# Optimization experiments

Hardware: AMD Instinct MI355X
Metric: run time of the kernel (lower is better)

Reference implementation:

```python
import jax, jax.numpy as jnp
import numpy as np

N_EMB = 1024
EMB_DIM = 256
BETA = 0.25


def setup_inputs() -> dict:
    key = jax.random.key(0)
    k1, k2 = jax.random.split(key)
    z = jax.random.normal(k1, (32, EMB_DIM, 32, 32), dtype=jnp.float32)
    init = 1.0 / N_EMB
    emb = jax.random.uniform(k2, (N_EMB, EMB_DIM), dtype=jnp.float32,
                             minval=-init, maxval=init)
    return {"z": z, "emb": emb}


def reference(z, emb):
    # z: [B, C, H, W] -> [B, H, W, C]
    zc = jnp.transpose(z, (0, 2, 3, 1))
    z_flat = zc.reshape(-1, EMB_DIM)  # [N, D]

    # squared L2 distances: ||z||^2 + ||e||^2 - 2 z.e^T  -> [N, K]
    distances = (jnp.sum(z_flat ** 2, axis=1, keepdims=True)
                 + jnp.sum(emb ** 2, axis=1)
                 - 2.0 * (z_flat @ emb.T))
    nearest_idx = jnp.argmin(distances, axis=1)           # [N]
    nearest = jax.nn.one_hot(nearest_idx, N_EMB, dtype=jnp.float32)  # [N, K]

    # direct gather == one-hot matmul, same math
    zq = emb[nearest_idx].reshape(zc.shape)               # [B, H, W, C]

    loss = (jnp.mean((jax.lax.stop_gradient(zq) - zc) ** 2)
            + BETA * jnp.mean((zq - jax.lax.stop_gradient(zc)) ** 2))

    # straight-through estimator
    zq_st = zc + jax.lax.stop_gradient(zq - zc)

    e_mean = jnp.mean(nearest, axis=0)                    # [K]
    perplexity = jnp.exp(-jnp.sum(e_mean * jnp.log(e_mean + 1e-10)))

    zq_out = jnp.transpose(zq_st, (0, 3, 1, 2))           # back to NCHW
    return zq_out, loss, perplexity, nearest, nearest_idx[:, None]
```

## Files before the change

### kernel.cpp

```cpp
#include <hip/hip_runtime.h>

#define N_EMB  1024
#define EMB_D  256
#define HW     1024

#define OUT_ZQ      0
#define OUT_LOSS    8388608
#define OUT_PERP    8388609
#define OUT_NEAREST 8388610
#define OUT_IDX     41943042

#define WS_HIST   0
#define WS_ESQ    4096
#define WS_LOSSP  8192
#define WS_EH     16384
#define WS_TOTAL  540672

typedef unsigned long long ull;
typedef _Float16 half8 __attribute__((ext_vector_type(8)));
typedef float f32x4 __attribute__((ext_vector_type(4)));
typedef ull ull2 __attribute__((ext_vector_type(2)));

#define L_A     0
#define L_B     16384
#define L_ESQ   32768
#define L_ZSQ   36864
#define L_WIN   36992
#define L_RED   37120
#define L_TOT   39168

__device__ __forceinline__ void gload16(const void* g, void* l) {
    __builtin_amdgcn_global_load_lds(
        (const __attribute__((address_space(1))) unsigned int*)g,
        (__attribute__((address_space(3))) unsigned int*)l, 16, 0, 0);
}

__device__ __forceinline__ float pairwise8_combine(const float r[8]) {
    return __fadd_rn(__fadd_rn(__fadd_rn(r[0], r[1]), __fadd_rn(r[2], r[3])),
                     __fadd_rn(__fadd_rn(r[4], r[5]), __fadd_rn(r[6], r[7])));
}

__global__ void prep(const float* __restrict__ emb, _Float16* __restrict__ eh,
                     float* __restrict__ esq, int* __restrict__ hist) {
    int bid = blockIdx.x;
    if (bid < 1024) {
        int c = bid, k = threadIdx.x;
        eh[c * EMB_D + k] = (_Float16)emb[c * EMB_D + k];
        return;
    }
    int c = (bid - 1024) * 256 + threadIdx.x;
    const float* p = emb + (size_t)c * EMB_D;
    float tot[2];
    #pragma unroll
    for (int h = 0; h < 2; ++h) {
        float r[8];
        #pragma unroll
        for (int i = 0; i < 8; ++i) {
            float x = p[h * 128 + i];
            r[i] = __fmul_rn(x, x);
        }
        for (int k = 8; k < 128; k += 8) {
            #pragma unroll
            for (int i = 0; i < 8; ++i) {
                float x = p[h * 128 + k + i];
                r[i] = __fadd_rn(r[i], __fmul_rn(x, x));
            }
        }
        tot[h] = pairwise8_combine(r);
    }
    esq[c] = __fadd_rn(tot[0], tot[1]);
    hist[c] = 0;
}

__global__ __launch_bounds__(256, 4) void fused_vq(
        const float* __restrict__ z, const float* __restrict__ emb,
        const _Float16* __restrict__ eh, const float* __restrict__ esq,
        float* __restrict__ out, int* __restrict__ hist,
        double* __restrict__ lossp) {
    __shared__ __align__(16) char lds[L_TOT];
    int t = threadIdx.x, bid = blockIdx.x;
    int b = bid >> 5, hw0 = (bid & 31) << 5;
    int lane = t & 63, wave = t >> 6;
    int wm = wave >> 1, wn = wave & 1;
    int l15 = lane & 15, lq = lane >> 4;

    if (t < 64) {
        int nl = t & 31, h = (t >> 5) & 1;
        const float* zp = z + ((size_t)b << 18) + hw0 + nl;
        int kb = h << 7;
        int abase = L_A + nl * 512;
        int sw = (nl & 7) << 4;
        float r[8];
        {   half8 hv;
            #pragma unroll
            for (int e = 0; e < 8; ++e) {
                float x = zp[(size_t)(kb + e) << 10];
                hv[e] = (_Float16)x;
                r[e] = __fmul_rn(x, x);
            }
            *(half8*)(lds + abase + (((kb << 1)) ^ sw)) = hv;
        }
        for (int c8 = 1; c8 < 16; ++c8) {
            half8 hv;
            #pragma unroll
            for (int e = 0; e < 8; ++e) {
                float x = zp[(size_t)(kb + c8 * 8 + e) << 10];
                hv[e] = (_Float16)x;
                r[e] = __fadd_rn(r[e], __fmul_rn(x, x));
            }
            *(half8*)(lds + abase + (((kb << 1) + c8 * 16) ^ sw)) = hv;
        }
        *(float*)(lds + L_RED + (h * 32 + nl) * 4) = pairwise8_combine(r);
    } else if (t >= 128) {
        int i = t - 128;
        #pragma unroll
        for (int q = 0; q < 2; ++q) {
            f32x4 v = *(const f32x4*)(esq + (q * 128 + i) * 4);
            *(f32x4*)(lds + L_ESQ + (q * 128 + i) * 16) = v;
        }
    }
    __syncthreads();
    if (t < 32) {
        float t0 = *(float*)(lds + L_RED + t * 4);
        float t1 = *(float*)(lds + L_RED + 128 + t * 4);
        *(float*)(lds + L_ZSQ + t * 4) = __fadd_rn(t0, t1);
    }
    __syncthreads();

    int aoffs[2], boffs[4][2];
    {
        int r = wm * 16 + l15;
        #pragma unroll
        for (int kc = 0; kc < 2; ++kc)
            aoffs[kc] = L_A + r * 512 + ((kc * 64 + lq * 16) ^ ((r & 7) << 4));
    }
    #pragma unroll
    for (int j = 0; j < 4; ++j) {
        int c = wn * 64 + j * 16 + l15;
        #pragma unroll
        for (int kc = 0; kc < 2; ++kc)
            boffs[j][kc] = L_B + c * 128 + ((kc * 64 + lq * 16) ^ ((c & 7) << 4));
    }
    int bsrc[4], bdst[4];
    #pragma unroll
    for (int is = 0; is < 4; ++is) {
        int o = is * 4096 + t * 16;
        int col = o >> 7;
        int K = (o & 127) ^ ((col & 7) << 4);
        bsrc[is] = col * 256 + (K >> 1);
        bdst[is] = L_B + o;
    }
    float zs[4];
    #pragma unroll
    for (int s = 0; s < 4; ++s)
        zs[s] = *(const float*)(lds + L_ZSQ + (wm * 16 + lq * 4 + s) * 4);
    ull k1[4], k2[4];
    #pragma unroll
    for (int s = 0; s < 4; ++s) { k1[s] = ~0ULL; k2[s] = ~0ULL; }

    for (int cbt = 0; cbt < 8; ++cbt) {
        f32x4 acc[4];
        #pragma unroll
        for (int j = 0; j < 4; ++j) acc[j] = (f32x4){0.f, 0.f, 0.f, 0.f};

        for (int kt = 0; kt < 4; ++kt) {
            __syncthreads();
            #pragma unroll
            for (int is = 0; is < 4; ++is)
                gload16(eh + cbt * 32768 + kt * 64 + bsrc[is], lds + bdst[is]);
            __syncthreads();

            half8 a0 = *(const half8*)(lds + aoffs[0] + kt * 128);
            half8 a1 = *(const half8*)(lds + aoffs[1] + kt * 128);
            half8 bb[4][2];
            #pragma unroll
            for (int j = 0; j < 4; ++j) {
                bb[j][0] = *(const half8*)(lds + boffs[j][0]);
                bb[j][1] = *(const half8*)(lds + boffs[j][1]);
            }
            #pragma unroll
            for (int j = 0; j < 4; ++j) {
                acc[j] = __builtin_amdgcn_mfma_f32_16x16x32_f16(a0, bb[j][0], acc[j], 0, 0, 0);
                acc[j] = __builtin_amdgcn_mfma_f32_16x16x32_f16(a1, bb[j][1], acc[j], 0, 0, 0);
            }
        }
        float es[4];
        #pragma unroll
        for (int j = 0; j < 4; ++j)
            es[j] = *(const float*)(lds + L_ESQ + ((cbt << 7) + wn * 64 + j * 16 + l15) * 4);
        #pragma unroll
        for (int s = 0; s < 4; ++s) {
            float zsv = zs[s];
            #pragma unroll
            for (int j = 0; j < 4; ++j) {
                float d = __fsub_rn(__fadd_rn(zsv, es[j]), __fmul_rn(2.0f, acc[j][s]));
                int cg = (cbt << 7) + wn * 64 + j * 16 + l15;
                ull key = ((ull)__float_as_uint(d) << 32) | (unsigned)cg;
                if (key < k1[s]) { k2[s] = k1[s]; k1[s] = key; }
                else if (key < k2[s]) { k2[s] = key; }
            }
        }
    }

    __syncthreads();
    #pragma unroll
    for (int s = 0; s < 4; ++s) {
        int row = wm * 16 + lq * 4 + s;
        *(ull2*)(lds + L_A + row * 512 + ((wn << 4) + l15) * 16) = (ull2){k1[s], k2[s]};
    }
    __syncthreads();

    for (int rr = 0; rr < 8; ++rr) {
        int row = wave * 8 + rr;
        ull k = *(const ull*)(lds + L_A + row * 512 + lane * 8);
        ull kmin = k;
        #pragma unroll
        for (int m = 1; m < 64; m <<= 1) {
            ull o = __shfl_xor(kmin, m, 64);
            kmin = o < kmin ? o : kmin;
        }
        float dmin = __uint_as_float((unsigned)(kmin >> 32));
        float dme  = __uint_as_float((unsigned)(k >> 32));
        bool cand = dme <= __fadd_rn(dmin, 2e-4f);
        ull bal = __ballot(cand);
        int winner;
        if (__popcll(bal) == 1) {
            winner = (int)(unsigned)(kmin & 0xFFFFFFFFu);
        } else {
            const float* zp2 = z + ((size_t)b << 18) + hw0 + row;
            float zr[4];
            #pragma unroll
            for (int e = 0; e < 4; ++e) zr[e] = zp2[(size_t)(lane + 64 * e) << 10];
            float zsr = *(const float*)(lds + L_ZSQ + row * 4);
            ull bestk = ~0ULL;
            while (bal) {
                int src = __ffsll(bal) - 1;
                bal &= bal - 1;
                ull ck = __shfl(k, src, 64);
                int c = (int)(unsigned)(ck & 0xFFFFFFFFu);
                const float* ep = emb + (size_t)c * EMB_D;
                float p = __fmul_rn(zr[3], ep[lane + 192]);
                p = __builtin_fmaf(zr[2], ep[lane + 128], p);
                p = __builtin_fmaf(zr[1], ep[lane + 64], p);
                p = __builtin_fmaf(zr[0], ep[lane], p);
                #pragma unroll
                for (int m = 1; m < 64; m <<= 1)
                    p = __fadd_rn(p, __shfl_xor(p, m, 64));
                float ec = *(const float*)(lds + L_ESQ + c * 4);
                float d = __fsub_rn(__fadd_rn(zsr, ec), __fmul_rn(2.0f, p));
                ull kk2 = ((ull)__float_as_uint(d) << 32) | (unsigned)c;
                bestk = kk2 < bestk ? kk2 : bestk;
            }
            winner = (int)(unsigned)(bestk & 0xFFFFFFFFu);
        }
        size_t n = (size_t)bid * 32 + row;
        float* np = out + OUT_NEAREST + (n << 10);
        #pragma unroll
        for (int q = 0; q < 4; ++q) {
            int c4 = q * 256 + lane * 4;
            f32x4 v = { winner == c4     ? 1.f : 0.f, winner == c4 + 1 ? 1.f : 0.f,
                        winner == c4 + 2 ? 1.f : 0.f, winner == c4 + 3 ? 1.f : 0.f };
            *(f32x4*)(np + c4) = v;
        }
        if (lane == 0) {
            out[OUT_IDX + n] = (float)winner;
            atomicAdd(&hist[winner], 1);
            *(int*)(lds + L_WIN + row * 4) = winner;
        }
    }
    __syncthreads();

    {
        int q = t & 7;
        int cq = t >> 3;
        int4 w4 = *(const int4*)(lds + L_WIN + q * 16);
        const float* zb = z + ((size_t)b << 18) + hw0 + q * 4;
        float* ob = out + OUT_ZQ + ((size_t)b << 18) + hw0 + q * 4;
        double s = 0.0;
        #pragma unroll
        for (int i = 0; i < 8; ++i) {
            int c = cq + (i << 5);
            f32x4 zc = *(const f32x4*)(zb + ((size_t)c << 10));
            f32x4 ev = { emb[(size_t)w4.x * EMB_D + c], emb[(size_t)w4.y * EMB_D + c],
                         emb[(size_t)w4.z * EMB_D + c], emb[(size_t)w4.w * EMB_D + c] };
            f32x4 df = { __fsub_rn(ev[0], zc[0]), __fsub_rn(ev[1], zc[1]),
                         __fsub_rn(ev[2], zc[2]), __fsub_rn(ev[3], zc[3]) };
            f32x4 st = { __fadd_rn(zc[0], df[0]), __fadd_rn(zc[1], df[1]),
                         __fadd_rn(zc[2], df[2]), __fadd_rn(zc[3], df[3]) };
            *(f32x4*)(ob + ((size_t)c << 10)) = st;
            s += (double)__fmul_rn(df[0], df[0]) + (double)__fmul_rn(df[1], df[1])
               + (double)__fmul_rn(df[2], df[2]) + (double)__fmul_rn(df[3], df[3]);
        }
        *(double*)(lds + L_RED + t * 8) = s;
        __syncthreads();
        for (int st = 128; st > 0; st >>= 1) {
            if (t < st) {
                double o = *(double*)(lds + L_RED + (t + st) * 8);
                *(double*)(lds + L_RED + t * 8) += o;
            }
            __syncthreads();
        }
        if (t == 0) lossp[bid] = *(double*)(lds + L_RED);
    }
}

__global__ void finalize_scalars(const double* __restrict__ lossp,
                                 const int* __restrict__ hist,
                                 float* __restrict__ out_loss,
                                 float* __restrict__ out_perp) {
    __shared__ double sd[1024];
    int t = threadIdx.x;

    sd[t] = lossp[t];
    __syncthreads();
    for (int st = 512; st > 0; st >>= 1) {
        if (t < st) sd[t] += sd[t + st];
        __syncthreads();
    }
    if (t == 0) {
        double loss = 1.25 * (sd[0] / 8388608.0);
        *out_loss = (float)loss;
    }
    __syncthreads();

    float p = (float)hist[t] * (1.0f / 32768.0f);
    float term = __fmul_rn(p, logf(__fadd_rn(p, 1e-10f)));
    sd[t] = (double)term;
    __syncthreads();
    for (int st = 512; st > 0; st >>= 1) {
        if (t < st) sd[t] += sd[t + st];
        __syncthreads();
    }
    if (t == 0) *out_perp = expf(-(float)sd[0]);
}

extern "C" void kernel_launch(void* const* d_in, const int* in_sizes, int n_in,
                              void* d_out, int out_size, void* d_ws, size_t ws_size,
                              hipStream_t stream) {
    const float* z   = (const float*)d_in[0];
    const float* emb = (const float*)d_in[1];
    float* out = (float*)d_out;
    char*  ws  = (char*)d_ws;

    int*      hist  = (int*)(ws + WS_HIST);
    float*    esq   = (float*)(ws + WS_ESQ);
    double*   lossp = (double*)(ws + WS_LOSSP);
    _Float16* eh    = (_Float16*)(ws + WS_EH);

    prep<<<1028, 256, 0, stream>>>(emb, eh, esq, hist);
    fused_vq<<<1024, 256, 0, stream>>>(z, emb, eh, esq, out, hist, lossp);
    finalize_scalars<<<1, 1024, 0, stream>>>(lossp, hist,
                                             out + OUT_LOSS, out + OUT_PERP);
}
```

Baseline: 82.08 us.

## Fold finalize into last fused block and vectorize codebook fp16 conversion

Removes the separate finalize_scalars launch by having the last fused_vq block, detected with an atomic counter and threadfence, reduce the loss partials and the histogram entropy. The prep kernel now converts the codebook to fp16 in 64 blocks using 16-element vector stores instead of 1024 scalar blocks, and it resets the counter. The A-fragment LDS reads are moved ahead of a barrier in the K loop. This saves launch and tail overhead at the cost of an extra global atomic per block and a serialized tail in one block.

```diff
diff --git a/kernel.cpp b/kernel.cpp
--- a/kernel.cpp
+++ b/kernel.cpp
@@ -13,8 +13,9 @@
 #define WS_HIST   0
 #define WS_ESQ    4096
 #define WS_LOSSP  8192
-#define WS_EH     16384
-#define WS_TOTAL  540672
+#define WS_CNT    16384
+#define WS_EH     16896
+#define WS_TOTAL  541184
 
 typedef unsigned long long ull;
 typedef _Float16 half8 __attribute__((ext_vector_type(8)));
@@ -41,14 +42,21 @@
 }
 
 __global__ void prep(const float* __restrict__ emb, _Float16* __restrict__ eh,
-                     float* __restrict__ esq, int* __restrict__ hist) {
+                     float* __restrict__ esq, int* __restrict__ hist,
+                     unsigned* __restrict__ cnt) {
     int bid = blockIdx.x;
-    if (bid < 1024) {
-        int c = bid, k = threadIdx.x;
-        eh[c * EMB_D + k] = (_Float16)emb[c * EMB_D + k];
+    if (bid < 64) {
+        int g = bid * 4096 + threadIdx.x * 16;
+        half8 h0, h1;
+        #pragma unroll
+        for (int e = 0; e < 8; ++e) h0[e] = (_Float16)emb[g + e];
+        #pragma unroll
+        for (int e = 0; e < 8; ++e) h1[e] = (_Float16)emb[g + 8 + e];
+        *(half8*)(eh + g) = h0;
+        *(half8*)(eh + g + 8) = h1;
         return;
     }
-    int c = (bid - 1024) * 256 + threadIdx.x;
+    int c = (bid - 64) * 256 + threadIdx.x;
     const float* p = emb + (size_t)c * EMB_D;
     float tot[2];
     #pragma unroll
@@ -70,14 +78,16 @@
     }
     esq[c] = __fadd_rn(tot[0], tot[1]);
     hist[c] = 0;
+    if (bid == 64 && threadIdx.x == 0) *cnt = 0;
 }
 
 __global__ __launch_bounds__(256, 4) void fused_vq(
         const float* __restrict__ z, const float* __restrict__ emb,
         const _Float16* __restrict__ eh, const float* __restrict__ esq,
         float* __restrict__ out, int* __restrict__ hist,
-        double* __restrict__ lossp) {
+        double* __restrict__ lossp, unsigned* __restrict__ cnt) {
     __shared__ __align__(16) char lds[L_TOT];
+    __shared__ unsigned lastflag;
     int t = threadIdx.x, bid = blockIdx.x;
     int b = bid >> 5, hw0 = (bid & 31) << 5;
     int lane = t & 63, wave = t >> 6;
@@ -168,10 +178,10 @@
             #pragma unroll
             for (int is = 0; is < 4; ++is)
                 gload16(eh + cbt * 32768 + kt * 64 + bsrc[is], lds + bdst[is]);
-            __syncthreads();
-
             half8 a0 = *(const half8*)(lds + aoffs[0] + kt * 128);
             half8 a1 = *(const half8*)(lds + aoffs[1] + kt * 128);
+            __syncthreads();
+
             half8 bb[4][2];
             #pragma unroll
             for (int j = 0; j < 4; ++j) {
@@ -302,36 +312,47 @@
         }
         if (t == 0) lossp[bid] = *(double*)(lds + L_RED);
     }
-}
-
-__global__ void finalize_scalars(const double* __restrict__ lossp,
-                                 const int* __restrict__ hist,
-                                 float* __restrict__ out_loss,
-                                 float* __restrict__ out_perp) {
-    __shared__ double sd[1024];
-    int t = threadIdx.x;
-
-    sd[t] = lossp[t];
-    __syncthreads();
-    for (int st = 512; st > 0; st >>= 1) {
-        if (t < st) sd[t] += sd[t + st];
+
+    __threadfence();
+    if (t == 0) lastflag = atomicAdd(cnt, 1u);
+    __syncthreads();
+    if (lastflag == 1023u) {
+        volatile double* lp = lossp;
+        double s = lp[t] + lp[t + 256] + lp[t + 512] + lp[t + 768];
+        *(double*)(lds + L_RED + t * 8) = s;
         __syncthreads();
-    }
-    if (t == 0) {
-        double loss = 1.25 * (sd[0] / 8388608.0);
-        *out_loss = (float)loss;
-    }
-    __syncthreads();
-
-    float p = (float)hist[t] * (1.0f / 32768.0f);
-    float term = __fmul_rn(p, logf(__fadd_rn(p, 1e-10f)));
-    sd[t] = (double)term;
-    __syncthreads();
-    for (int st = 512; st > 0; st >>= 1) {
-        if (t < st) sd[t] += sd[t + st];
+        for (int st = 128; st > 0; st >>= 1) {
+            if (t < st) {
+                double o = *(double*)(lds + L_RED + (t + st) * 8);
+                *(double*)(lds + L_RED + t * 8) += o;
+            }
+            __syncthreads();
+        }
+        if (t == 0) {
+            double loss = 1.25 * ((*(double*)(lds + L_RED)) / 8388608.0);
+            out[OUT_LOSS] = (float)loss;
+        }
         __syncthreads();
-    }
-    if (t == 0) *out_perp = expf(-(float)sd[0]);
+
+        volatile int* hv = hist;
+        double ps = 0.0;
+        #pragma unroll
+        for (int qh = 0; qh < 4; ++qh) {
+            float p = (float)hv[t + qh * 256] * (1.0f / 32768.0f);
+            float term = __fmul_rn(p, logf(__fadd_rn(p, 1e-10f)));
+            ps += (double)term;
+        }
+        *(double*)(lds + L_RED + t * 8) = ps;
+        __syncthreads();
+        for (int st = 128; st > 0; st >>= 1) {
+            if (t < st) {
+                double o = *(double*)(lds + L_RED + (t + st) * 8);
+                *(double*)(lds + L_RED + t * 8) += o;
+            }
+            __syncthreads();
+        }
+        if (t == 0) out[OUT_PERP] = expf(-(float)(*(double*)(lds + L_RED)));
+    }
 }
 
 extern "C" void kernel_launch(void* const* d_in, const int* in_sizes, int n_in,
@@ -345,10 +366,9 @@
     int*      hist  = (int*)(ws + WS_HIST);
     float*    esq   = (float*)(ws + WS_ESQ);
     double*   lossp = (double*)(ws + WS_LOSSP);
+    unsigned* cnt   = (unsigned*)(ws + WS_CNT);
     _Float16* eh    = (_Float16*)(ws + WS_EH);
 
-    prep<<<1028, 256, 0, stream>>>(emb, eh, esq, hist);
-    fused_vq<<<1024, 256, 0, stream>>>(z, emb, eh, esq, out, hist, lossp);
-    finalize_scalars<<<1, 1024, 0, stream>>>(lossp, hist,
-                                             out + OUT_LOSS, out + OUT_PERP);
-}
+    prep<<<68, 256, 0, stream>>>(emb, eh, esq, hist, cnt);
+    fused_vq<<<1024, 256, 0, stream>>>(z, emb, eh, esq, out, hist, lossp, cnt);
+}
```

New measurement: 251.7 us. +206.7%, slower.

## Split fused VQ kernel into argmin and output-write kernels, vectorize fp16 prep

Applied to the files above, without the earlier changes.

Splits the fused kernel into two. vq_argmin computes the nearest code indices and histogram and stores the indices in workspace. vq_write then emits the one-hot matrix, the straight-through output and the loss partials. The aim is to free the compute-heavy argmin kernel from the large output writes and its extra LDS, which may improve occupancy and scheduling. The prep kernel also converts the embedding to fp16 with vectorized 16-element-per-thread stores over 64 blocks instead of 1024 scalar blocks. The cost is an extra kernel launch, an index round trip through global memory, and z and emb being re-read in the second kernel.

```diff
diff --git a/kernel.cpp b/kernel.cpp
--- a/kernel.cpp
+++ b/kernel.cpp
@@ -13,8 +13,9 @@
 #define WS_HIST   0
 #define WS_ESQ    4096
 #define WS_LOSSP  8192
-#define WS_EH     16384
-#define WS_TOTAL  540672
+#define WS_IDX    16384
+#define WS_EH     147456
+#define WS_TOTAL  671744
 
 typedef unsigned long long ull;
 typedef _Float16 half8 __attribute__((ext_vector_type(8)));
@@ -25,9 +26,8 @@
 #define L_B     16384
 #define L_ESQ   32768
 #define L_ZSQ   36864
-#define L_WIN   36992
-#define L_RED   37120
-#define L_TOT   39168
+#define L_RED   36992
+#define L_TOT   37504
 
 __device__ __forceinline__ void gload16(const void* g, void* l) {
     __builtin_amdgcn_global_load_lds(
@@ -43,12 +43,18 @@
 __global__ void prep(const float* __restrict__ emb, _Float16* __restrict__ eh,
                      float* __restrict__ esq, int* __restrict__ hist) {
     int bid = blockIdx.x;
-    if (bid < 1024) {
-        int c = bid, k = threadIdx.x;
-        eh[c * EMB_D + k] = (_Float16)emb[c * EMB_D + k];
+    if (bid < 64) {
+        int g = bid * 4096 + threadIdx.x * 16;
+        half8 h0, h1;
+        #pragma unroll
+        for (int e = 0; e < 8; ++e) h0[e] = (_Float16)emb[g + e];
+        #pragma unroll
+        for (int e = 0; e < 8; ++e) h1[e] = (_Float16)emb[g + 8 + e];
+        *(half8*)(eh + g) = h0;
+        *(half8*)(eh + g + 8) = h1;
         return;
     }
-    int c = (bid - 1024) * 256 + threadIdx.x;
+    int c = (bid - 64) * 256 + threadIdx.x;
     const float* p = emb + (size_t)c * EMB_D;
     float tot[2];
     #pragma unroll
@@ -72,11 +78,11 @@
     hist[c] = 0;
 }
 
-__global__ __launch_bounds__(256, 4) void fused_vq(
+__global__ __launch_bounds__(256, 4) void vq_argmin(
         const float* __restrict__ z, const float* __restrict__ emb,
         const _Float16* __restrict__ eh, const float* __restrict__ esq,
-        float* __restrict__ out, int* __restrict__ hist,
-        double* __restrict__ lossp) {
+        int* __restrict__ idxarr, float* __restrict__ out_idx,
+        int* __restrict__ hist) {
     __shared__ __align__(16) char lds[L_TOT];
     int t = threadIdx.x, bid = blockIdx.x;
     int b = bid >> 5, hw0 = (bid & 31) << 5;
@@ -253,8 +259,32 @@
             }
             winner = (int)(unsigned)(bestk & 0xFFFFFFFFu);
         }
-        size_t n = (size_t)bid * 32 + row;
-        float* np = out + OUT_NEAREST + (n << 10);
+        if (lane == 0) {
+            size_t n = (size_t)bid * 32 + row;
+            idxarr[n] = winner;
+            out_idx[n] = (float)winner;
+            atomicAdd(&hist[winner], 1);
+        }
+    }
+}
+
+__global__ __launch_bounds__(256) void vq_write(
+        const float* __restrict__ z, const float* __restrict__ emb,
+        const int* __restrict__ idxarr, float* __restrict__ out,
+        double* __restrict__ lossp) {
+    __shared__ __align__(16) int win[32];
+    __shared__ double red[256];
+    int t = threadIdx.x, bid = blockIdx.x;
+    int b = bid >> 5, hw0 = (bid & 31) << 5;
+    int lane = t & 63, wave = t >> 6;
+
+    if (t < 32) win[t] = idxarr[bid * 32 + t];
+    __syncthreads();
+
+    for (int rr = 0; rr < 8; ++rr) {
+        int row = wave * 8 + rr;
+        int winner = win[row];
+        float* np = out + OUT_NEAREST + (((size_t)bid * 32 + row) << 10);
         #pragma unroll
         for (int q = 0; q < 4; ++q) {
             int c4 = q * 256 + lane * 4;
@@ -262,18 +292,12 @@
                         winner == c4 + 2 ? 1.f : 0.f, winner == c4 + 3 ? 1.f : 0.f };
             *(f32x4*)(np + c4) = v;
         }
-        if (lane == 0) {
-            out[OUT_IDX + n] = (float)winner;
-            atomicAdd(&hist[winner], 1);
-            *(int*)(lds + L_WIN + row * 4) = winner;
-        }
-    }
-    __syncthreads();
+    }
 
     {
         int q = t & 7;
         int cq = t >> 3;
-        int4 w4 = *(const int4*)(lds + L_WIN + q * 16);
+        int4 w4 = *(const int4*)(win + q * 4);
         const float* zb = z + ((size_t)b << 18) + hw0 + q * 4;
         float* ob = out + OUT_ZQ + ((size_t)b << 18) + hw0 + q * 4;
         double s = 0.0;
@@ -291,16 +315,13 @@
             s += (double)__fmul_rn(df[0], df[0]) + (double)__fmul_rn(df[1], df[1])
                + (double)__fmul_rn(df[2], df[2]) + (double)__fmul_rn(df[3], df[3]);
         }
-        *(double*)(lds + L_RED + t * 8) = s;
+        red[t] = s;
         __syncthreads();
         for (int st = 128; st > 0; st >>= 1) {
-            if (t < st) {
-                double o = *(double*)(lds + L_RED + (t + st) * 8);
-                *(double*)(lds + L_RED + t * 8) += o;
-            }
+            if (t < st) red[t] += red[t + st];
             __syncthreads();
         }
-        if (t == 0) lossp[bid] = *(double*)(lds + L_RED);
+        if (t == 0) lossp[bid] = red[0];
     }
 }
 
@@ -342,13 +363,16 @@
     float* out = (float*)d_out;
     char*  ws  = (char*)d_ws;
 
-    int*      hist  = (int*)(ws + WS_HIST);
-    float*    esq   = (float*)(ws + WS_ESQ);
-    double*   lossp = (double*)(ws + WS_LOSSP);
-    _Float16* eh    = (_Float16*)(ws + WS_EH);
-
-    prep<<<1028, 256, 0, stream>>>(emb, eh, esq, hist);
-    fused_vq<<<1024, 256, 0, stream>>>(z, emb, eh, esq, out, hist, lossp);
+    int*      hist   = (int*)(ws + WS_HIST);
+    float*    esq    = (float*)(ws + WS_ESQ);
+    double*   lossp  = (double*)(ws + WS_LOSSP);
+    int*      idxarr = (int*)(ws + WS_IDX);
+    _Float16* eh     = (_Float16*)(ws + WS_EH);
+
+    prep<<<68, 256, 0, stream>>>(emb, eh, esq, hist);
+    vq_argmin<<<1024, 256, 0, stream>>>(z, emb, eh, esq, idxarr,
+                                        out + OUT_IDX, hist);
+    vq_write<<<1024, 256, 0, stream>>>(z, emb, idxarr, out, lossp);
     finalize_scalars<<<1, 1024, 0, stream>>>(lossp, hist,
                                              out + OUT_LOSS, out + OUT_PERP);
 }
```

Result: slower. 91.31 us (+11.2%).
